# Performance work log

Measured on AMD Instinct MI355X. Metric: run time of the kernel, lower is better.

Reference implementation:

```python
import jax, jax.numpy as jnp
import numpy as np

B, D, H, E, TOPK = 8192, 1024, 4096, 8, 2


def setup_inputs() -> dict:
    key = jax.random.key(0)
    ks = jax.random.split(key, 5)
    s_in = 1.0 / np.sqrt(D)
    s_h = 1.0 / np.sqrt(H)
    return {
        "x": jax.random.normal(ks[0], (B, D), jnp.float32),
        "Wg": jax.random.normal(ks[1], (D, E), jnp.float32) * s_in,
        "bg": jnp.zeros((E,), jnp.float32),
        "W1": jax.random.normal(ks[2], (E, D, H), jnp.float32) * s_in,
        "b1": jnp.zeros((E, H), jnp.float32),
        "W2": jax.random.normal(ks[3], (E, H, D), jnp.float32) * s_h,
        "b2": jnp.zeros((E, D), jnp.float32),
    }


def reference(x, Wg, bg, W1, b1, W2, b2):
    # Gating: softmax over experts, top-k, renormalize selected weights
    logits = x @ Wg + bg                              # [B, E]
    weights = jax.nn.softmax(logits, axis=-1)
    topw, topi = jax.lax.top_k(weights, TOPK)         # [B, k]
    topw = topw / jnp.sum(topw, axis=-1, keepdims=True)
    # Dense combine weights: [B, E], zero for unselected experts
    comb = jnp.sum(topw[..., None] * jax.nn.one_hot(topi, E, dtype=x.dtype), axis=1)
    # Expert MLPs computed batched per expert (grouped GEMM form)
    h = jax.nn.gelu(jnp.einsum('bd,edh->ebh', x, W1) + b1[:, None, :], approximate=False)  # [E,B,H]
    y = jnp.einsum('ebh,ehd->ebd', h, W2) + b2[:, None, :]                                 # [E,B,D]
    # Weighted combine: only top-k experts have nonzero weight
    out = jnp.einsum('ebd,be->bd', y, comb)           # [B, D]
    return out
```

## Files before the change

kernel.cpp:

```cpp
#include <hip/hip_runtime.h>
#include <stdint.h>

#define B_TOK 8192
#define DDIM 1024
#define HDIM 4096
#define NEXP 8
#define MAXTILE 72

typedef __bf16 bf16x8 __attribute__((ext_vector_type(8)));
typedef float f32x4 __attribute__((ext_vector_type(4)));

__device__ __forceinline__ unsigned short f2bf(float f) {
  unsigned int u = __float_as_uint(f);
  u += 0x7fffu + ((u >> 16) & 1u);
  return (unsigned short)(u >> 16);
}
__device__ __forceinline__ float bfhi(unsigned int u) {
  return __uint_as_float(u & 0xffff0000u);
}
__device__ __forceinline__ float bflo(unsigned int u) {
  return __uint_as_float(u << 16);
}

__device__ __forceinline__ void gld16(const void* g, void* l) {
  __builtin_amdgcn_global_load_lds(
      (const __attribute__((address_space(1))) void*)g,
      (__attribute__((address_space(3))) void*)l, 16, 0, 0);
}

__device__ __forceinline__ float gelu_f(float v) {
  float u = v * (0.7978845608f + 0.0356774081f * v * v);
  float ex = __expf(2.f * u);
  float th = 1.f - 2.f * __builtin_amdgcn_rcpf(ex + 1.f);
  return 0.5f * v * (1.f + th);
}

__global__ __launch_bounds__(256) void gating_kernel(
    const float* __restrict__ x, const float* __restrict__ Wg,
    const float* __restrict__ bg, int* __restrict__ t2e,
    float* __restrict__ t2w, int* __restrict__ cnt,
    unsigned short* __restrict__ xb) {
  __shared__ float sWg[NEXP * DDIM];
  int tid = threadIdx.x;
  for (int i = tid; i < NEXP * DDIM; i += 256) {
    int d = i >> 3, e = i & 7;
    sWg[e * DDIM + d] = Wg[i];
  }
  __syncthreads();
  int lane = tid & 63, wave = tid >> 6;
  for (int t = 0; t < 16; ++t) {
    int b = blockIdx.x * 64 + wave * 16 + t;
    float acc[NEXP];
#pragma unroll
    for (int e = 0; e < NEXP; ++e) acc[e] = 0.f;
    const float* xr = x + (size_t)b * DDIM;
    unsigned short* xw = xb + (size_t)b * DDIM;
#pragma unroll
    for (int j = 0; j < 4; ++j) {
      int d0 = j * 256 + lane * 4;
      float4 xv = *(const float4*)(xr + d0);
      ushort4 o;
      o.x = f2bf(xv.x); o.y = f2bf(xv.y); o.z = f2bf(xv.z); o.w = f2bf(xv.w);
      *(ushort4*)(xw + d0) = o;
#pragma unroll
      for (int e = 0; e < NEXP; ++e) {
        float4 wv = *(const float4*)(sWg + e * DDIM + d0);
        acc[e] += xv.x * wv.x + xv.y * wv.y + xv.z * wv.z + xv.w * wv.w;
      }
    }
#pragma unroll
    for (int off = 32; off > 0; off >>= 1) {
#pragma unroll
      for (int e = 0; e < NEXP; ++e) acc[e] += __shfl_xor(acc[e], off);
    }
    if (lane == 0) {
      float l0[NEXP];
#pragma unroll
      for (int e = 0; e < NEXP; ++e) l0[e] = acc[e] + bg[e];
      int i1 = 0;
      float v1 = l0[0];
#pragma unroll
      for (int e = 1; e < NEXP; ++e)
        if (l0[e] > v1) { v1 = l0[e]; i1 = e; }
      int i2 = (i1 == 0) ? 1 : 0;
      float v2 = l0[i2];
#pragma unroll
      for (int e = 0; e < NEXP; ++e)
        if (e != i1 && l0[e] > v2) { v2 = l0[e]; i2 = e; }
      float w1 = 1.f / (1.f + expf(v2 - v1));
      float w2 = 1.f - w1;
      t2e[b * 2] = i1;
      t2e[b * 2 + 1] = i2;
      t2w[b * 2] = w1;
      t2w[b * 2 + 1] = w2;
      atomicAdd(&cnt[i1], 1);
      atomicAdd(&cnt[i2], 1);
    }
  }
}

__global__ void prefix_kernel(const int* __restrict__ cnt, int* __restrict__ offs,
                              int* __restrict__ tileE, int* __restrict__ tileM,
                              int* __restrict__ ntile) {
  int s = 0, t = 0;
  offs[0] = 0;
  for (int e = 0; e < NEXP; ++e) {
    int c = cnt[e];
    for (int m = 0; m < c; m += 256) { tileE[t] = e; tileM[t] = m; ++t; }
    s += c;
    offs[e + 1] = s;
  }
  *ntile = t;
}

__global__ __launch_bounds__(256) void scatter_kernel(
    const int* __restrict__ t2e, const int* __restrict__ offs,
    int* __restrict__ cursor, int* __restrict__ tok, int* __restrict__ rowpos) {
  __shared__ int lcnt[NEXP], lbase[NEXP];
  int tid = threadIdx.x;
  if (tid < NEXP) lcnt[tid] = 0;
  __syncthreads();
  int b = blockIdx.x * 256 + tid;
  int e0 = t2e[b * 2], e1 = t2e[b * 2 + 1];
  int i0 = atomicAdd(&lcnt[e0], 1);
  int i1 = atomicAdd(&lcnt[e1], 1);
  __syncthreads();
  if (tid < NEXP) lbase[tid] = atomicAdd(&cursor[tid], lcnt[tid]);
  __syncthreads();
  int p0 = offs[e0] + lbase[e0] + i0;
  int p1 = offs[e1] + lbase[e1] + i1;
  tok[p0] = b;
  tok[p1] = b;
  rowpos[b * 2] = p0;
  rowpos[b * 2 + 1] = p1;
}

__global__ __launch_bounds__(256) void transpose_cvt_kernel(
    const float* __restrict__ src, unsigned short* __restrict__ dst, int R, int C) {
  __shared__ unsigned short T[64][72];
  size_t eo = (size_t)blockIdx.z * (size_t)R * C;
  int c0 = blockIdx.x * 64, r0 = blockIdx.y * 64;
  int tid = threadIdx.x;
#pragma unroll
  for (int p = 0; p < 4; ++p) {
    int idx = p * 256 + tid;
    int r = idx >> 4, c4 = (idx & 15) * 4;
    float4 v = *(const float4*)(src + eo + (size_t)(r0 + r) * C + c0 + c4);
    T[r][c4] = f2bf(v.x);
    T[r][c4 + 1] = f2bf(v.y);
    T[r][c4 + 2] = f2bf(v.z);
    T[r][c4 + 3] = f2bf(v.w);
  }
  __syncthreads();
#pragma unroll
  for (int p = 0; p < 2; ++p) {
    int idx = p * 256 + tid;
    int c = idx >> 3, s8 = (idx & 7) * 8;
    ushort4 a, b;
    a.x = T[s8][c];     a.y = T[s8 + 1][c]; a.z = T[s8 + 2][c]; a.w = T[s8 + 3][c];
    b.x = T[s8 + 4][c]; b.y = T[s8 + 5][c]; b.z = T[s8 + 6][c]; b.w = T[s8 + 7][c];
    unsigned short* dp = dst + eo + (size_t)(c0 + c) * R + r0 + s8;
    *(ushort4*)dp = a;
    *(ushort4*)(dp + 4) = b;
  }
}

#define BAR() __builtin_amdgcn_s_barrier()
#define SB() __builtin_amdgcn_sched_barrier(0)
#define LG0() asm volatile("s_waitcnt lgkmcnt(0)" ::: "memory")
#define VMW(n) asm volatile("s_waitcnt vmcnt(" #n ")" ::: "memory")
#define RGN(t, mat, ks) (&LDS[(t) & 1][mat][ks][0][0])
#define STAGE(mat, P0p, P1p, t, ks)                                 \
  do {                                                              \
    unsigned short* _d = RGN(t, mat, ks) + wave * 512;              \
    gld16((P0p) + (size_t)(t) * 64 + (ks) * 32, _d);                \
    gld16((P1p) + (size_t)(t) * 64 + (ks) * 32, _d + 4096);         \
  } while (0)
#define RDA_TO(dst, t, ks)                                          \
  do {                                                              \
    const unsigned short* _p = RGN(t, 0, ks);                       \
    _Pragma("unroll") for (int n = 0; n < 4; ++n)                   \
        dst[n] = *(const bf16x8*)(_p + aoff[n]);                    \
  } while (0)
#define RDB_TO(dst, t, ks, h)                                       \
  do {                                                              \
    const unsigned short* _p = RGN(t, 1, ks);                       \
    _Pragma("unroll") for (int m = 0; m < 4; ++m)                   \
        dst[m] = *(const bf16x8*)(_p + boff2[h][m]);                \
  } while (0)
#define MMQ2(Av, Bv, h)                                             \
  do {                                                              \
    __builtin_amdgcn_s_setprio(1);                                  \
    _Pragma("unroll") for (int i = 0; i < 4; ++i)                   \
        _Pragma("unroll") for (int j = 0; j < 4; ++j)               \
            acc[i][(h)*4 + j] = __builtin_amdgcn_mfma_f32_16x16x32_bf16( \
                Av[i], Bv[j], acc[i][(h)*4 + j], 0, 0, 0);          \
    __builtin_amdgcn_s_setprio(0);                                  \
  } while (0)

template <int KD, bool GELU, bool GATHER>
__global__ __launch_bounds__(512, 2) void moe_gemm(
    const unsigned short* __restrict__ Bsrc, const unsigned short* __restrict__ Wt,
    const float* __restrict__ bias, const int* __restrict__ offs,
    const int* __restrict__ tileE, const int* __restrict__ tileM,
    const int* __restrict__ ntile, const int* __restrict__ tok,
    unsigned short* __restrict__ obuf, int ND) {
  constexpr int NT = KD / 64;
  static_assert(NT >= 3, "pipeline needs >=3 K-tiles");
  __shared__ __attribute__((aligned(16))) unsigned short LDS[2][2][2][256][32];
  int ty = blockIdx.y;
  if (ty >= *ntile) return;
  int e = tileE[ty], m0 = tileM[ty];
  int r0 = offs[e], rows = offs[e + 1] - r0;
  int n0 = blockIdx.x * 256;
  int tid = threadIdx.x, lane = tid & 63, wave = tid >> 6;
  int wn = wave & 3, wm = wave >> 2;
  int nbase = wn * 64, mbase = wm * 128;
  int fr = lane & 15, quad = lane >> 4;

  int rs = tid >> 2;
  int ss = (tid & 3) ^ ((rs >> 1) & 3);
  const unsigned short* pA0 = Wt + ((size_t)e * ND + n0 + rs) * KD + ss * 8;
  const unsigned short* pA1 = pA0 + (size_t)128 * KD;
  int mr0 = min(m0 + rs, rows - 1), mr1 = min(m0 + 128 + rs, rows - 1);
  size_t br0, br1;
  if constexpr (GATHER) {
    br0 = (size_t)tok[r0 + mr0];
    br1 = (size_t)tok[r0 + mr1];
  } else {
    br0 = (size_t)(r0 + mr0);
    br1 = (size_t)(r0 + mr1);
  }
  const unsigned short* pB0 = Bsrc + br0 * KD + ss * 8;
  const unsigned short* pB1 = Bsrc + br1 * KD + ss * 8;

  int aoff[4], boff2[2][4];
#pragma unroll
  for (int n = 0; n < 4; ++n) {
    int rA = nbase + n * 16 + fr;
    aoff[n] = rA * 32 + (quad ^ ((rA >> 1) & 3)) * 8;
  }
#pragma unroll
  for (int h = 0; h < 2; ++h)
#pragma unroll
    for (int m = 0; m < 4; ++m) {
      int rB = mbase + h * 64 + m * 16 + fr;
      boff2[h][m] = rB * 32 + (quad ^ ((rB >> 1) & 3)) * 8;
    }

  f32x4 acc[4][8];
#pragma unroll
  for (int i = 0; i < 4; ++i)
#pragma unroll
    for (int j = 0; j < 8; ++j) acc[i][j] = (f32x4){0.f, 0.f, 0.f, 0.f};
  bf16x8 aE[4], aO[4], bE[4], bO[4];

  STAGE(0, pA0, pA1, 0, 0);
  STAGE(1, pB0, pB1, 0, 0);
  STAGE(0, pA0, pA1, 0, 1);
  STAGE(1, pB0, pB1, 0, 1);
  STAGE(0, pA0, pA1, 1, 0);
  STAGE(1, pB0, pB1, 1, 0);
  STAGE(0, pA0, pA1, 1, 1);
  VMW(10);
  BAR();
  RDA_TO(aE, 0, 0);
  RDB_TO(bE, 0, 0, 0);
  LG0();
  SB();

  for (int t = 0; t < NT - 2; ++t) {
    RDB_TO(bO, t, 0, 1);
    STAGE(1, pB0, pB1, t + 1, 1);
    SB();
    MMQ2(aE, bE, 0);
    SB();
    VMW(8); LG0(); SB();
    BAR();
    RDA_TO(aO, t, 1);
    RDB_TO(bE, t, 1, 0);
    STAGE(0, pA0, pA1, t + 2, 0);
    SB();
    MMQ2(aE, bO, 1);
    SB();
    LG0(); SB();
    BAR();
    RDB_TO(bO, t, 1, 1);
    STAGE(1, pB0, pB1, t + 2, 0);
    SB();
    MMQ2(aO, bE, 0);
    SB();
    VMW(8); LG0(); SB();
    BAR();
    RDA_TO(aE, t + 1, 0);
    RDB_TO(bE, t + 1, 0, 0);
    STAGE(0, pA0, pA1, t + 2, 1);
    SB();
    MMQ2(aO, bO, 1);
    SB();
    LG0(); SB();
    BAR();
  }
  {
    int t = NT - 2;
    RDB_TO(bO, t, 0, 1);
    STAGE(1, pB0, pB1, t + 1, 1);
    SB(); MMQ2(aE, bE, 0); SB();
    VMW(8); LG0(); SB();
    BAR();
    RDA_TO(aO, t, 1);
    RDB_TO(bE, t, 1, 0);
    SB(); MMQ2(aE, bO, 1); SB();
    LG0(); SB();
    BAR();
    RDB_TO(bO, t, 1, 1);
    SB(); MMQ2(aO, bE, 0); SB();
    VMW(4); LG0(); SB();
    BAR();
    RDA_TO(aE, t + 1, 0);
    RDB_TO(bE, t + 1, 0, 0);
    SB(); MMQ2(aO, bO, 1); SB();
    LG0(); SB();
    BAR();
  }
  {
    int t = NT - 1;
    RDB_TO(bO, t, 0, 1);
    SB(); MMQ2(aE, bE, 0); SB();
    VMW(0); LG0(); SB();
    BAR();
    RDA_TO(aO, t, 1);
    RDB_TO(bE, t, 1, 0);
    SB(); MMQ2(aE, bO, 1); SB();
    LG0(); SB();
    BAR();
    RDB_TO(bO, t, 1, 1);
    SB(); MMQ2(aO, bE, 0); SB();
    LG0(); SB();
    BAR();
    SB(); MMQ2(aO, bO, 1); SB();
  }

  const float* be = bias + (size_t)e * ND + n0 + nbase;
  float4 bv[4];
#pragma unroll
  for (int i = 0; i < 4; ++i) bv[i] = *(const float4*)(be + i * 16 + quad * 4);
#pragma unroll
  for (int j = 0; j < 8; ++j) {
    int grow = m0 + mbase + (j >> 2) * 64 + (j & 3) * 16 + fr;
    if (grow < rows) {
      unsigned short* yp = obuf + (size_t)(r0 + grow) * ND + n0 + nbase;
#pragma unroll
      for (int i = 0; i < 4; ++i) {
        float v0 = acc[i][j][0] + bv[i].x;
        float v1 = acc[i][j][1] + bv[i].y;
        float v2 = acc[i][j][2] + bv[i].z;
        float v3 = acc[i][j][3] + bv[i].w;
        if constexpr (GELU) {
          v0 = gelu_f(v0); v1 = gelu_f(v1); v2 = gelu_f(v2); v3 = gelu_f(v3);
        }
        ushort4 o;
        o.x = f2bf(v0); o.y = f2bf(v1); o.z = f2bf(v2); o.w = f2bf(v3);
        *(ushort4*)(yp + i * 16 + quad * 4) = o;
      }
    }
  }
}

__global__ __launch_bounds__(256) void combine_kernel(
    const unsigned short* __restrict__ ybuf, const int* __restrict__ rowpos,
    const float* __restrict__ t2w, float* __restrict__ out) {
  int idx = blockIdx.x * 256 + threadIdx.x;
  int b = idx >> 7;
  int c8 = (idx & 127) * 8;
  int p0 = rowpos[b * 2], p1 = rowpos[b * 2 + 1];
  float w0 = t2w[b * 2], w1 = t2w[b * 2 + 1];
  uint4 ya = *(const uint4*)(ybuf + (size_t)p0 * DDIM + c8);
  uint4 yb = *(const uint4*)(ybuf + (size_t)p1 * DDIM + c8);
  float4 o0, o1;
  o0.x = w0 * bflo(ya.x) + w1 * bflo(yb.x);
  o0.y = w0 * bfhi(ya.x) + w1 * bfhi(yb.x);
  o0.z = w0 * bflo(ya.y) + w1 * bflo(yb.y);
  o0.w = w0 * bfhi(ya.y) + w1 * bfhi(yb.y);
  o1.x = w0 * bflo(ya.z) + w1 * bflo(yb.z);
  o1.y = w0 * bfhi(ya.z) + w1 * bfhi(yb.z);
  o1.z = w0 * bflo(ya.w) + w1 * bflo(yb.w);
  o1.w = w0 * bfhi(ya.w) + w1 * bfhi(yb.w);
  float* op = out + (size_t)b * DDIM + c8;
  *(float4*)op = o0;
  *(float4*)(op + 4) = o1;
}

extern "C" void kernel_launch(void* const* d_in, const int* in_sizes, int n_in,
                              void* d_out, int out_size, void* d_ws, size_t ws_size,
                              hipStream_t stream) {
  const float* x = (const float*)d_in[0];
  const float* Wg = (const float*)d_in[1];
  const float* bg = (const float*)d_in[2];
  const float* W1 = (const float*)d_in[3];
  const float* b1 = (const float*)d_in[4];
  const float* W2 = (const float*)d_in[5];
  const float* b2 = (const float*)d_in[6];
  float* out = (float*)d_out;

  char* ws = (char*)d_ws;
  int* cnt = (int*)(ws + 0);
  int* cursor = (int*)(ws + 64);
  int* offs = (int*)(ws + 128);
  int* ntile = (int*)(ws + 192);
  int* tileE = (int*)(ws + 256);
  int* tileM = (int*)(ws + 896);
  int* t2e = (int*)(ws + 2048);
  float* t2w = (float*)(ws + 67584);
  int* tok = (int*)(ws + 133120);
  int* rowpos = (int*)(ws + 198656);
  char* big = ws + 264192;
  unsigned short* xb = (unsigned short*)big;
  unsigned short* w1t = (unsigned short*)(big + 16777216);
  unsigned short* ybuf = w1t;
  unsigned short* w2t = (unsigned short*)(big + 16777216 + 67108864);
  unsigned short* hbuf = (unsigned short*)(big + 16777216 + 2 * 67108864);

  (void)in_sizes; (void)n_in; (void)out_size; (void)ws_size;

  hipMemsetAsync(ws, 0, 256, stream);

  transpose_cvt_kernel<<<dim3(HDIM / 64, DDIM / 64, NEXP), 256, 0, stream>>>(W1, w1t, DDIM, HDIM);
  transpose_cvt_kernel<<<dim3(DDIM / 64, HDIM / 64, NEXP), 256, 0, stream>>>(W2, w2t, HDIM, DDIM);
  gating_kernel<<<B_TOK / 64, 256, 0, stream>>>(x, Wg, bg, t2e, t2w, cnt, xb);
  prefix_kernel<<<1, 1, 0, stream>>>(cnt, offs, tileE, tileM, ntile);
  scatter_kernel<<<B_TOK / 256, 256, 0, stream>>>(t2e, offs, cursor, tok, rowpos);
  moe_gemm<DDIM, true, true><<<dim3(HDIM / 256, MAXTILE), 512, 0, stream>>>(
      xb, w1t, b1, offs, tileE, tileM, ntile, tok, hbuf, HDIM);
  moe_gemm<HDIM, false, false><<<dim3(DDIM / 256, MAXTILE), 512, 0, stream>>>(
      hbuf, w2t, b2, offs, tileE, tileM, ntile, tok, ybuf, DDIM);
  combine_kernel<<<(B_TOK * DDIM) / (256 * 8), 256, 0, stream>>>(ybuf, rowpos, t2w, out);
}
```

Baseline: 904.3 us.

## Fuse both expert GEMMs into a persistent work-queue kernel with dependency flags

Replaces the two separate grouped-GEMM launches with a single persistent kernel of 256 blocks. Each block pulls work items from an atomic queue: first-layer tiles come first, then second-layer tiles that spin-wait on per-tile and per-expert completion counters. The aim is to remove the tail bubble between the two GEMMs and let the second layer start while the first is still finishing. In exchange it adds spin-wait synchronisation, a risk of stalls, and fixed occupancy. The gating kernel is also relaunched with twice as many blocks, each handling half the tokens.

After: 1.003 ms. +11.0%, slower.

```diff
diff --git a/kernel.cpp b/kernel.cpp
--- a/kernel.cpp
+++ b/kernel.cpp
@@ -48,8 +48,8 @@
   }
   __syncthreads();
   int lane = tid & 63, wave = tid >> 6;
-  for (int t = 0; t < 16; ++t) {
-    int b = blockIdx.x * 64 + wave * 16 + t;
+  for (int t = 0; t < 8; ++t) {
+    int b = blockIdx.x * 32 + wave * 8 + t;
     float acc[NEXP];
 #pragma unroll
     for (int e = 0; e < NEXP; ++e) acc[e] = 0.f;
@@ -101,12 +101,14 @@
 
 __global__ void prefix_kernel(const int* __restrict__ cnt, int* __restrict__ offs,
                               int* __restrict__ tileE, int* __restrict__ tileM,
-                              int* __restrict__ ntile) {
+                              int* __restrict__ ntile, int* __restrict__ g1cnt) {
   int s = 0, t = 0;
   offs[0] = 0;
   for (int e = 0; e < NEXP; ++e) {
     int c = cnt[e];
+    int t0 = t;
     for (int m = 0; m < c; m += 256) { tileE[t] = e; tileM[t] = m; ++t; }
+    g1cnt[e] = 16 * (t - t0);
     s += c;
     offs[e + 1] = s;
   }
@@ -198,21 +200,16 @@
     __builtin_amdgcn_s_setprio(0);                                  \
   } while (0)
 
-template <int KD, bool GELU, bool GATHER>
-__global__ __launch_bounds__(512, 2) void moe_gemm(
+typedef unsigned short LdsT[2][2][2][256][32];
+
+template <int NT, bool GELU, bool GATHER>
+__device__ __forceinline__ void run_tile(
     const unsigned short* __restrict__ Bsrc, const unsigned short* __restrict__ Wt,
-    const float* __restrict__ bias, const int* __restrict__ offs,
-    const int* __restrict__ tileE, const int* __restrict__ tileM,
-    const int* __restrict__ ntile, const int* __restrict__ tok,
-    unsigned short* __restrict__ obuf, int ND) {
-  constexpr int NT = KD / 64;
+    const float* __restrict__ bias, const int* __restrict__ tok,
+    unsigned short* __restrict__ obuf, int ND,
+    int e, int m0, int r0, int rows, int n0, LdsT& LDS) {
+  constexpr int KD = NT * 64;
   static_assert(NT >= 3, "pipeline needs >=3 K-tiles");
-  __shared__ __attribute__((aligned(16))) unsigned short LDS[2][2][2][256][32];
-  int ty = blockIdx.y;
-  if (ty >= *ntile) return;
-  int e = tileE[ty], m0 = tileM[ty];
-  int r0 = offs[e], rows = offs[e + 1] - r0;
-  int n0 = blockIdx.x * 256;
   int tid = threadIdx.x, lane = tid & 63, wave = tid >> 6;
   int wn = wave & 3, wm = wave >> 2;
   int nbase = wn * 64, mbase = wm * 128;
@@ -363,6 +360,63 @@
         o.x = f2bf(v0); o.y = f2bf(v1); o.z = f2bf(v2); o.w = f2bf(v3);
         *(ushort4*)(yp + i * 16 + quad * 4) = o;
       }
+    }
+  }
+}
+
+__global__ __launch_bounds__(512, 2) void moe_fused(
+    const unsigned short* __restrict__ xb, const unsigned short* __restrict__ w1t,
+    const float* __restrict__ b1, const unsigned short* __restrict__ w2t,
+    const float* __restrict__ b2, const int* __restrict__ offs,
+    const int* __restrict__ tileE, const int* __restrict__ tileM,
+    const int* __restrict__ ntile, const int* __restrict__ tok,
+    const int* __restrict__ g1cnt, unsigned short* __restrict__ hbuf,
+    unsigned short* __restrict__ ybuf, int* __restrict__ qhead,
+    int* __restrict__ done, int* __restrict__ done1E) {
+  __shared__ __attribute__((aligned(16))) unsigned short LDS[2][2][2][256][32];
+  __shared__ int s_it;
+  int nt = *ntile;
+  int n1 = nt * 16;
+  int nall = n1 + nt * 4;
+  int tid = threadIdx.x;
+  for (;;) {
+    __syncthreads();
+    if (tid == 0) s_it = atomicAdd(qhead, 1);
+    __syncthreads();
+    int it = s_it;
+    if (it >= nall) return;
+    if (it < n1) {
+      int ty = it >> 4, nx = it & 15;
+      int e = tileE[ty], m0 = tileM[ty];
+      int r0 = offs[e], rows = offs[e + 1] - r0;
+      run_tile<DDIM / 64, true, true>(xb, w1t, b1, tok, hbuf, HDIM, e, m0, r0, rows,
+                                      nx * 256, LDS);
+      __syncthreads();
+      if (tid == 0) {
+        __hip_atomic_fetch_add(&done[ty], 1, __ATOMIC_RELEASE, __HIP_MEMORY_SCOPE_AGENT);
+        __hip_atomic_fetch_add(&done1E[e], 1, __ATOMIC_RELEASE, __HIP_MEMORY_SCOPE_AGENT);
+      }
+    } else {
+      int q = it - n1;
+      int ty = q >> 2, nx = q & 3;
+      int e = tileE[ty], m0 = tileM[ty];
+      int r0 = offs[e], rows = offs[e + 1] - r0;
+      if (tid == 0) {
+        while (__hip_atomic_load(&done[ty], __ATOMIC_RELAXED, __HIP_MEMORY_SCOPE_AGENT) < 16)
+          __builtin_amdgcn_s_sleep(2);
+        int eA = (r0 + m0) >> 12;
+        int eB = (r0 + m0 + 255) >> 12;
+        while (__hip_atomic_load(&done1E[eA], __ATOMIC_RELAXED, __HIP_MEMORY_SCOPE_AGENT) <
+               g1cnt[eA])
+          __builtin_amdgcn_s_sleep(2);
+        while (__hip_atomic_load(&done1E[eB], __ATOMIC_RELAXED, __HIP_MEMORY_SCOPE_AGENT) <
+               g1cnt[eB])
+          __builtin_amdgcn_s_sleep(2);
+        (void)__hip_atomic_load(&done[ty], __ATOMIC_ACQUIRE, __HIP_MEMORY_SCOPE_AGENT);
+      }
+      __syncthreads();
+      run_tile<HDIM / 64, false, false>(hbuf, w2t, b2, tok, ybuf, DDIM, e, m0, r0, rows,
+                                        nx * 256, LDS);
     }
   }
 }
@@ -408,8 +462,12 @@
   int* cursor = (int*)(ws + 64);
   int* offs = (int*)(ws + 128);
   int* ntile = (int*)(ws + 192);
-  int* tileE = (int*)(ws + 256);
-  int* tileM = (int*)(ws + 896);
+  int* qhead = (int*)(ws + 196);
+  int* done = (int*)(ws + 256);
+  int* done1E = (int*)(ws + 544);
+  int* g1cnt = (int*)(ws + 576);
+  int* tileE = (int*)(ws + 640);
+  int* tileM = (int*)(ws + 960);
   int* t2e = (int*)(ws + 2048);
   float* t2w = (float*)(ws + 67584);
   int* tok = (int*)(ws + 133120);
@@ -423,16 +481,14 @@
 
   (void)in_sizes; (void)n_in; (void)out_size; (void)ws_size;
 
-  hipMemsetAsync(ws, 0, 256, stream);
+  hipMemsetAsync(ws, 0, 1280, stream);
 
   transpose_cvt_kernel<<<dim3(HDIM / 64, DDIM / 64, NEXP), 256, 0, stream>>>(W1, w1t, DDIM, HDIM);
   transpose_cvt_kernel<<<dim3(DDIM / 64, HDIM / 64, NEXP), 256, 0, stream>>>(W2, w2t, HDIM, DDIM);
-  gating_kernel<<<B_TOK / 64, 256, 0, stream>>>(x, Wg, bg, t2e, t2w, cnt, xb);
-  prefix_kernel<<<1, 1, 0, stream>>>(cnt, offs, tileE, tileM, ntile);
+  gating_kernel<<<B_TOK / 32, 256, 0, stream>>>(x, Wg, bg, t2e, t2w, cnt, xb);
+  prefix_kernel<<<1, 1, 0, stream>>>(cnt, offs, tileE, tileM, ntile, g1cnt);
   scatter_kernel<<<B_TOK / 256, 256, 0, stream>>>(t2e, offs, cursor, tok, rowpos);
-  moe_gemm<DDIM, true, true><<<dim3(HDIM / 256, MAXTILE), 512, 0, stream>>>(
-      xb, w1t, b1, offs, tileE, tileM, ntile, tok, hbuf, HDIM);
-  moe_gemm<HDIM, false, false><<<dim3(DDIM / 256, MAXTILE), 512, 0, stream>>>(
-      hbuf, w2t, b2, offs, tileE, tileM, ntile, tok, ybuf, DDIM);
+  moe_fused<<<256, 512, 0, stream>>>(xb, w1t, b1, w2t, b2, offs, tileE, tileM, ntile,
+                                     tok, g1cnt, hbuf, ybuf, qhead, done, done1E);
   combine_kernel<<<(B_TOK * DDIM) / (256 * 8), 256, 0, stream>>>(ybuf, rowpos, t2w, out);
 }
```
